# Performance work log

Measured on AMD Instinct MI355X. Metric: run time of the kernel, lower is better.

The kernel has to match this reference:

```python
import jax, jax.numpy as jnp
import numpy as np

MEM = 32      # mem_size == slot_size (required by role/mem einsum contraction)
SLOT = 32
NREAD = 1
NITER = 3
NIN = 3       # num_input
EPS = 1e-8


def _ln(x, g=None, b=None, eps=1e-5):
    m = x.mean(-1, keepdims=True)
    v = x.var(-1, keepdims=True)
    y = (x - m) / jnp.sqrt(v + eps)
    if g is not None:
        y = y * g + b
    return y


def _lstm_layer(x, Wih, Whh, bih, bhh):
    # x: [S, B, Din]; torch gate order i, f, g, o
    B = x.shape[1]
    H = Whh.shape[1]
    def step(carry, xt):
        h, c = carry
        z = xt @ Wih.T + h @ Whh.T + bih + bhh
        i, f, g, o = jnp.split(z, 4, axis=-1)
        c = jax.nn.sigmoid(f) * c + jax.nn.sigmoid(i) * jnp.tanh(g)
        h = jax.nn.sigmoid(o) * jnp.tanh(c)
        return (h, c), h
    init = (jnp.zeros((B, H), x.dtype), jnp.zeros((B, H), x.dtype))
    _, hs = jax.lax.scan(step, init, x)
    return hs


def _slot_attention(inp, inp_cat, Wi, bi, Wq, bq, Wk, bk, Wv, bv, lng, lnb,
                    Wm1, bm1, Wm2, bm2, Wsp, bsp):
    # inp: [S, B, NIN, 64]; dropout is identity (eval)
    S, B = inp.shape[0], inp.shape[1]
    init_slots = (inp_cat @ Wi.T + bi).reshape(S, B, -1, SLOT)
    k = jax.nn.elu(inp @ Wk.T + bk) + 1.0
    v = inp @ Wv.T + bv
    slots = init_slots
    for _ in range(NITER):
        q = (slots @ Wq.T + bq + init_slots) * SLOT ** (-0.5)
        q = jax.nn.elu(q) + 1.0
        logits = jnp.einsum('sbik,sbjk->sbij', k, q)
        attn = jax.nn.softmax(logits, axis=3) + EPS
        attn = attn / attn.sum(axis=2, keepdims=True)
        upd = jnp.einsum('sbij,sbik->sbjk', attn, v)
        h = _ln(upd, lng, lnb)
        mlp = jax.nn.relu(h @ Wm1.T + bm1) @ Wm2.T + bm2
        slots = slots + mlp / SLOT
    slots = jnp.concatenate([init_slots, slots], axis=-1)
    return slots @ Wsp.T + bsp


def _mask_read(slots, mask, i):
    return jnp.tanh(jnp.einsum('sbne,n->sbe', slots, jnp.roll(mask, i)))


def setup_inputs() -> dict:
    key = jax.random.key(0)
    ks = jax.random.split(key, 20)
    def n(k, shape):
        return jax.random.normal(k, shape, jnp.float32) * 0.05
    z = lambda s: jnp.zeros(s, jnp.float32)
    return {
        'tokens': jax.random.randint(ks[0], (512, 64), 0, 32000),
        'embed_W': n(ks[1], (32000, 256)),
        'Wih0': n(ks[2], (2048, 256)), 'Whh0': n(ks[3], (2048, 512)),
        'bih0': z(2048), 'bhh0': z(2048),
        'Wih1': n(ks[4], (2048, 512)), 'Whh1': n(ks[5], (2048, 512)),
        'bih1': z(2048), 'bhh1': z(2048),
        'Wpi': n(ks[6], (192, 256)), 'bpi': z(192),
        'Wq': n(ks[7], (32, 32)), 'bq': z(32),
        'Wk': n(ks[8], (32, 64)), 'bk': z(32),
        'Wv': n(ks[9], (32, 64)), 'bv': z(32),
        'lng': jnp.ones(32, jnp.float32), 'lnb': z(32),
        'Wm1': n(ks[10], (64, 32)), 'bm1': z(64),
        'Wm2': n(ks[11], (32, 64)), 'bm2': z(32),
        'Wbind': n(ks[12], (96, 192)), 'bbind': z(96),
        'Wreas': n(ks[13], (64, 192)), 'breas': z(64),
        'Wsp': n(ks[14], (32, 64)), 'bsp': z(32),
        'Wg': n(ks[15], (1, 512)), 'bg': z(1),
        'Wout': n(ks[16], (128, 544)), 'bout': z(128),
    }


def reference(tokens, embed_W, Wih0, Whh0, bih0, bhh0, Wih1, Whh1, bih1, bhh1,
              Wpi, bpi, Wq, bq, Wk, bk, Wv, bv, lng, lnb, Wm1, bm1, Wm2, bm2,
              Wbind, bbind, Wreas, breas, Wsp, bsp, Wg, bg, Wout, bout):
    S, B = tokens.shape
    emb = embed_W[tokens]                                   # [S,B,256]
    h = _lstm_layer(emb, Wih0, Whh0, bih0, bhh0)            # [S,B,512]
    h = _lstm_layer(h, Wih1, Whh1, bih1, bhh1)
    dec_in = (emb @ Wpi.T + bpi).reshape(S, B, NIN, -1)     # [S,B,3,64]
    dec_cat = dec_in.reshape(S, B, -1)
    sa = (Wq, bq, Wk, bk, Wv, bv, lng, lnb, Wm1, bm1, Wm2, bm2, Wsp, bsp)
    bind_slots = _slot_attention(dec_in, dec_cat, Wbind, bbind, *sa)  # [S,B,3,32]
    reas_slots = _slot_attention(dec_in, dec_cat, Wreas, breas, *sa)  # [S,B,2,32]
    e = 1e-6
    mask_b = jnp.array([1.0 - 2 * e, e, e], emb.dtype)
    role1 = _mask_read(bind_slots, mask_b, 0)
    role2 = _mask_read(bind_slots, mask_b, 1)
    filler = _mask_read(bind_slots, mask_b, 2)
    mask_r = jnp.array([1.0 - (1 + NREAD) * e, e], emb.dtype)
    u1 = _mask_read(reas_slots, mask_r, 0)
    u2 = _mask_read(reas_slots, mask_r, 1)
    gate = jax.nn.sigmoid(h @ Wg.T + bg + 1.0)              # [S,B,1]

    def step(mem, xs):
        r1, r2, f, g_t, u1t, u2t = xs
        role = jnp.einsum('br,bt->brt', r1, r2)
        prev = jnp.einsum('brt,brtf->bf', role, mem)
        cur = g_t * (f - prev)
        mem = mem + jnp.einsum('brt,bf->brtf', role, cur / MEM)
        nrm = jnp.sqrt(jnp.sum(mem * mem, axis=(1, 2, 3)))
        nrm = jax.nn.relu(nrm - 1.0) + 1.0
        mem = mem / nrm[:, None, None, None]
        read = _ln(jnp.einsum('bsrv,bs,br->bv', mem, u1t, u2t))
        return mem, read

    mem0 = jnp.zeros((B, MEM, MEM, MEM), emb.dtype)
    _, reads = jax.lax.scan(step, mem0, (role1, role2, filler, gate, u1, u2))
    out = jnp.concatenate([h, reads], axis=-1) @ Wout.T + bout
    return out
```

## Files before the change

kernel.cpp:

```cpp
#include <hip/hip_runtime.h>

typedef unsigned short u16;
typedef unsigned int u32;
typedef unsigned long long u64;
typedef __bf16 bf16x8 __attribute__((ext_vector_type(8)));
typedef float f32x4 __attribute__((ext_vector_type(4)));

__device__ __forceinline__ float bf2f(u16 u) { return __uint_as_float(((u32)u) << 16); }
__device__ __forceinline__ u16 f2bf(float f) {
    u32 u = __float_as_uint(f);
    u32 r = (u + 0x7FFFu + ((u >> 16) & 1u)) >> 16;
    return (u16)r;
}
__device__ __forceinline__ float sigm(float x) { return 1.0f / (1.0f + __expf(-x)); }
__device__ __forceinline__ float elu1(float x) { return x > 0.0f ? x + 1.0f : __expf(x); }

__device__ __forceinline__ void wb() { __builtin_amdgcn_wave_barrier(); }

__device__ __forceinline__ int ag_load(const int* p) {
    return __hip_atomic_load(p, __ATOMIC_RELAXED, __HIP_MEMORY_SCOPE_AGENT);
}
__device__ __forceinline__ void ag_store(int* p, int v) {
    __hip_atomic_store(p, v, __ATOMIC_RELAXED, __HIP_MEMORY_SCOPE_AGENT);
}
__device__ __forceinline__ void llc_store2(u16* p, u16 a, u16 b) {
    u32 v = (u32)a | ((u32)b << 16);
    __hip_atomic_store((u32*)p, v, __ATOMIC_RELAXED, __HIP_MEMORY_SCOPE_AGENT);
}
__device__ __forceinline__ void llc_store_u16(u16* p, u16 v) {
    __hip_atomic_store(p, v, __ATOMIC_RELAXED, __HIP_MEMORY_SCOPE_AGENT);
}

struct Cvt8 { const float* s[8]; u16* d[8]; int off4[9]; };

__global__ __launch_bounds__(256) void k_f2b8(Cvt8 c)
{
    int i = blockIdx.x * 256 + threadIdx.x;
    if (i >= c.off4[8]) return;
    int k = 0;
#pragma unroll
    for (int q = 1; q < 8; q++) if (i >= c.off4[q]) k = q;
    int j = i - c.off4[k];
    float4 v = ((const float4*)c.s[k])[j];
    ushort4 o;
    o.x = f2bf(v.x); o.y = f2bf(v.y); o.z = f2bf(v.z); o.w = f2bf(v.w);
    ((ushort4*)c.d[k])[j] = o;
}

__global__ __launch_bounds__(256) void k_embed(const int* __restrict__ tok,
                                               const float* __restrict__ W,
                                               u16* __restrict__ out)
{
    int c = blockIdx.x * 256 + threadIdx.x;
    int row = c >> 5, cc = (c & 31) * 8;
    int t = tok[row];
    const float* src = W + (size_t)t * 256 + cc;
    u16 tmp[8];
#pragma unroll
    for (int k = 0; k < 8; k++) tmp[k] = f2bf(src[k]);
    *(uint4*)(out + (size_t)row * 256 + cc) = *(uint4*)tmp;
}

__global__ __launch_bounds__(256) void k_gemm_bt(
    const u16* __restrict__ A, int lda,
    const u16* __restrict__ B,
    u16* __restrict__ Cb, float* __restrict__ Cf, int ldc,
    const float* __restrict__ bias1, const float* __restrict__ bias2,
    int N, int K)
{
    __shared__ u16 As[128][40];
    __shared__ u16 Bs[128][40];
    const int tid = threadIdx.x;
    const int m0 = blockIdx.x * 128, n0 = blockIdx.y * 128;
    const int wave = tid >> 6, lane = tid & 63;
    const int wm = wave & 1, wn = wave >> 1;
    const int quad = lane >> 4, l16 = lane & 15;
    f32x4 acc[4][4] = {};
    for (int k0 = 0; k0 < K; k0 += 32) {
        __syncthreads();
#pragma unroll
        for (int i = 0; i < 2; i++) {
            int c = tid + i * 256, row = c >> 2, cc = (c & 3) * 8;
            *(uint4*)(&As[row][cc]) = *(const uint4*)(A + (size_t)(m0 + row) * lda + k0 + cc);
            uint4 d = {0, 0, 0, 0};
            if (n0 + row < N) d = *(const uint4*)(B + (size_t)(n0 + row) * K + k0 + cc);
            *(uint4*)(&Bs[row][cc]) = d;
        }
        __syncthreads();
        bf16x8 af[4], bfm[4];
#pragma unroll
        for (int x = 0; x < 4; x++) {
            af[x]  = *(const bf16x8*)(&As[wm * 64 + x * 16 + l16][quad * 8]);
            bfm[x] = *(const bf16x8*)(&Bs[wn * 64 + x * 16 + l16][quad * 8]);
        }
#pragma unroll
        for (int mi = 0; mi < 4; mi++)
#pragma unroll
            for (int ni = 0; ni < 4; ni++)
                acc[mi][ni] = __builtin_amdgcn_mfma_f32_16x16x32_bf16(af[mi], bfm[ni], acc[mi][ni], 0, 0, 0);
    }
#pragma unroll
    for (int ni = 0; ni < 4; ni++) {
        int col = n0 + wn * 64 + ni * 16 + l16;
        if (col < N) {
            float bv = 0.f;
            if (bias1) bv += bias1[col];
            if (bias2) bv += bias2[col];
#pragma unroll
            for (int mi = 0; mi < 4; mi++) {
                int r0 = m0 + wm * 64 + mi * 16 + quad * 4;
#pragma unroll
                for (int r = 0; r < 4; r++) {
                    float v = acc[mi][ni][r] + bv;
                    if (Cb) Cb[(size_t)(r0 + r) * ldc + col] = f2bf(v);
                    else    Cf[(size_t)(r0 + r) * ldc + col] = v;
                }
            }
        }
    }
}

struct SmemSlot {
    float WqT[32][33], WkT[64][33], WvT[64][33], Wm1T[32][65], Wm2T[64][33], WspT[64][33];
    float bq[32], bk[32], bv[32], bm1[64], bm2[32], bsp[32], g[32], be[32];
    u16 xbuf[8][192];
    float slots[8][3][32], initl[8][3][32], kk[8][3][32], vv[8][3][32], qq[8][3][32];
    float att[8][3][4];
    float ubuf[8][32];
    float hid[8][64];
};

__device__ __forceinline__ void stage_slot_weights(SmemSlot& S, const int tid,
    const float* __restrict__ Wq, const float* __restrict__ bq,
    const float* __restrict__ Wk, const float* __restrict__ bk,
    const float* __restrict__ Wv, const float* __restrict__ bv,
    const float* __restrict__ lng, const float* __restrict__ lnb,
    const float* __restrict__ Wm1, const float* __restrict__ bm1,
    const float* __restrict__ Wm2, const float* __restrict__ bm2,
    const float* __restrict__ Wsp, const float* __restrict__ bsp)
{
    for (int i = tid; i < 1024; i += 256) { int o = i >> 5, c = i & 31; S.WqT[c][o] = Wq[o * 32 + c]; }
    for (int i = tid; i < 2048; i += 256) {
        int o6 = i >> 6, c6 = i & 63;
        S.WkT[c6][o6]  = Wk[o6 * 64 + c6];
        S.WvT[c6][o6]  = Wv[o6 * 64 + c6];
        S.Wm2T[c6][o6] = Wm2[o6 * 64 + c6];
        S.WspT[c6][o6] = Wsp[o6 * 64 + c6];
        int o5 = i >> 5, c5 = i & 31;
        S.Wm1T[c5][o5] = Wm1[o5 * 32 + c5];
    }
    if (tid < 32) {
        S.bq[tid] = bq[tid]; S.bk[tid] = bk[tid]; S.bv[tid] = bv[tid];
        S.bm2[tid] = bm2[tid]; S.bsp[tid] = bsp[tid];
        S.g[tid] = lng[tid]; S.be[tid] = lnb[tid];
    }
    if (tid < 64) S.bm1[tid] = bm1[tid];
}

template <int NSLOT>
__device__ __forceinline__ void slot_unit(
    SmemSlot& S, const int tid, const size_t row0,
    const u16* __restrict__ dec, const u16* __restrict__ initp,
    float* __restrict__ o1, float* __restrict__ o2, float* __restrict__ o3)
{
    const int p = tid >> 5, l = tid & 31;
    const size_t row = row0 + p;
    for (int i = l; i < 192; i += 32) S.xbuf[p][i] = dec[row * 192 + i];
    wb();
#pragma unroll
    for (int i = 0; i < 3; i++) {
        float k0 = 0.f, k1 = 0.f, v0 = 0.f, v1 = 0.f;
#pragma unroll
        for (int c = 0; c < 64; c += 4) {
            float x0 = bf2f(S.xbuf[p][i * 64 + c]);
            float x1 = bf2f(S.xbuf[p][i * 64 + c + 1]);
            float x2 = bf2f(S.xbuf[p][i * 64 + c + 2]);
            float x3 = bf2f(S.xbuf[p][i * 64 + c + 3]);
            float wk0 = S.WkT[c][l], wk1 = S.WkT[c + 1][l];
            float wk2 = S.WkT[c + 2][l], wk3 = S.WkT[c + 3][l];
            float wv0 = S.WvT[c][l], wv1 = S.WvT[c + 1][l];
            float wv2 = S.WvT[c + 2][l], wv3 = S.WvT[c + 3][l];
            k0 += x0 * wk0; k1 += x1 * wk1; k0 += x2 * wk2; k1 += x3 * wk3;
            v0 += x0 * wv0; v1 += x1 * wv1; v0 += x2 * wv2; v1 += x3 * wv3;
        }
        S.kk[p][i][l] = elu1(S.bk[l] + (k0 + k1));
        S.vv[p][i][l] = S.bv[l] + (v0 + v1);
    }
#pragma unroll
    for (int j = 0; j < NSLOT; j++) {
        float iv = bf2f(initp[row * (NSLOT * 32) + j * 32 + l]);
        S.initl[p][j][l] = iv;
        S.slots[p][j][l] = iv;
    }
    wb();
    const float rs = 0.17677669529663687f;
    for (int it = 0; it < 3; it++) {
#pragma unroll
        for (int j = 0; j < NSLOT; j++) {
            float a0 = 0.f, a1 = 0.f, a2 = 0.f, a3 = 0.f;
#pragma unroll
            for (int c = 0; c < 32; c += 4) {
                float s0 = S.slots[p][j][c],     s1 = S.slots[p][j][c + 1];
                float s2 = S.slots[p][j][c + 2], s3 = S.slots[p][j][c + 3];
                float w0 = S.WqT[c][l],     w1 = S.WqT[c + 1][l];
                float w2 = S.WqT[c + 2][l], w3 = S.WqT[c + 3][l];
                a0 += s0 * w0; a1 += s1 * w1; a2 += s2 * w2; a3 += s3 * w3;
            }
            S.qq[p][j][l] = elu1((S.bq[l] + ((a0 + a1) + (a2 + a3)) + S.initl[p][j][l]) * rs);
        }
        wb();
        if (l < 3 * NSLOT) {
            int i = l / NSLOT, j = l % NSLOT;
            float a0 = 0.f, a1 = 0.f, a2 = 0.f, a3 = 0.f;
#pragma unroll
            for (int c = 0; c < 32; c += 4) {
                a0 += S.kk[p][i][c]     * S.qq[p][j][c];
                a1 += S.kk[p][i][c + 1] * S.qq[p][j][c + 1];
                a2 += S.kk[p][i][c + 2] * S.qq[p][j][c + 2];
                a3 += S.kk[p][i][c + 3] * S.qq[p][j][c + 3];
            }
            S.att[p][i][j] = (a0 + a1) + (a2 + a3);
        }
        wb();
        if (l < 3) {
            float mx = -1e30f;
            for (int j = 0; j < NSLOT; j++) mx = fmaxf(mx, S.att[p][l][j]);
            float sm = 0.f, ex[3];
            for (int j = 0; j < NSLOT; j++) { ex[j] = __expf(S.att[p][l][j] - mx); sm += ex[j]; }
            for (int j = 0; j < NSLOT; j++) S.att[p][l][j] = ex[j] / sm + 1e-8f;
        }
        wb();
        if (l < NSLOT) {
            float s = S.att[p][0][l] + S.att[p][1][l] + S.att[p][2][l];
            float inv = 1.0f / s;
            for (int i = 0; i < 3; i++) S.att[p][i][l] *= inv;
        }
        wb();
#pragma unroll
        for (int j = 0; j < NSLOT; j++) {
            float u = S.att[p][0][j] * S.vv[p][0][l] + S.att[p][1][j] * S.vv[p][1][l] + S.att[p][2][j] * S.vv[p][2][l];
            float mean = u;
            for (int mk = 1; mk < 32; mk <<= 1) mean += __shfl_xor(mean, mk, 32);
            mean *= (1.0f / 32.0f);
            float d = u - mean;
            float var = d * d;
            for (int mk = 1; mk < 32; mk <<= 1) var += __shfl_xor(var, mk, 32);
            var *= (1.0f / 32.0f);
            float y = d * rsqrtf(var + 1e-5f) * S.g[l] + S.be[l];
            S.ubuf[p][l] = y;
            wb();
#pragma unroll
            for (int oo = 0; oo < 2; oo++) {
                int o = l + oo * 32;
                float a0 = 0.f, a1 = 0.f, a2 = 0.f, a3 = 0.f;
#pragma unroll
                for (int c = 0; c < 32; c += 4) {
                    float u0 = S.ubuf[p][c],     u1v_ = S.ubuf[p][c + 1];
                    float u2v_ = S.ubuf[p][c + 2], u3 = S.ubuf[p][c + 3];
                    float w0 = S.Wm1T[c][o],     w1 = S.Wm1T[c + 1][o];
                    float w2 = S.Wm1T[c + 2][o], w3 = S.Wm1T[c + 3][o];
                    a0 += u0 * w0; a1 += u1v_ * w1; a2 += u2v_ * w2; a3 += u3 * w3;
                }
                S.hid[p][o] = fmaxf(S.bm1[o] + ((a0 + a1) + (a2 + a3)), 0.f);
            }
            wb();
            float a0 = 0.f, a1 = 0.f, a2 = 0.f, a3 = 0.f;
#pragma unroll
            for (int c = 0; c < 64; c += 4) {
                float h0 = S.hid[p][c],     h1 = S.hid[p][c + 1];
                float h2 = S.hid[p][c + 2], h3 = S.hid[p][c + 3];
                float w0 = S.Wm2T[c][l],     w1 = S.Wm2T[c + 1][l];
                float w2 = S.Wm2T[c + 2][l], w3 = S.Wm2T[c + 3][l];
                a0 += h0 * w0; a1 += h1 * w1; a2 += h2 * w2; a3 += h3 * w3;
            }
            S.slots[p][j][l] += (S.bm2[l] + ((a0 + a1) + (a2 + a3))) * (1.0f / 32.0f);
            wb();
        }
    }
    float pj[NSLOT];
#pragma unroll
    for (int j = 0; j < NSLOT; j++) {
        float a0 = 0.f, a1 = 0.f, a2 = 0.f, a3 = 0.f;
#pragma unroll
        for (int c = 0; c < 32; c += 4) {
            float i0 = S.initl[p][j][c],     i1 = S.initl[p][j][c + 1];
            float i2 = S.initl[p][j][c + 2], i3 = S.initl[p][j][c + 3];
            float w0 = S.WspT[c][l],     w1 = S.WspT[c + 1][l];
            float w2 = S.WspT[c + 2][l], w3 = S.WspT[c + 3][l];
            a0 += i0 * w0; a1 += i1 * w1; a2 += i2 * w2; a3 += i3 * w3;
        }
#pragma unroll
        for (int c = 0; c < 32; c += 4) {
            float s0 = S.slots[p][j][c],     s1 = S.slots[p][j][c + 1];
            float s2 = S.slots[p][j][c + 2], s3 = S.slots[p][j][c + 3];
            float w0 = S.WspT[32 + c][l],     w1 = S.WspT[32 + c + 1][l];
            float w2 = S.WspT[32 + c + 2][l], w3 = S.WspT[32 + c + 3][l];
            a0 += s0 * w0; a1 += s1 * w1; a2 += s2 * w2; a3 += s3 * w3;
        }
        pj[j] = S.bsp[l] + ((a0 + a1) + (a2 + a3));
    }
    const float e = 1e-6f, me = (float)(1.0 - 2e-6);
    if (NSLOT == 3) {
        o1[row * 32 + l] = tanhf(me * pj[0] + e * pj[1] + e * pj[2]);
        o2[row * 32 + l] = tanhf(e * pj[0] + me * pj[1] + e * pj[2]);
        o3[row * 32 + l] = tanhf(e * pj[0] + e * pj[1] + me * pj[2]);
    } else {
        o1[row * 32 + l] = tanhf(me * pj[0] + e * pj[1]);
        o2[row * 32 + l] = tanhf(e * pj[0] + me * pj[1]);
    }
}

__global__ __launch_bounds__(256) void k_slotsweep(
    const u16* __restrict__ dec,
    const u16* __restrict__ initb, const u16* __restrict__ initr,
    const float* __restrict__ Wq, const float* __restrict__ bq,
    const float* __restrict__ Wk, const float* __restrict__ bk,
    const float* __restrict__ Wv, const float* __restrict__ bv,
    const float* __restrict__ lng, const float* __restrict__ lnb,
    const float* __restrict__ Wm1, const float* __restrict__ bm1,
    const float* __restrict__ Wm2, const float* __restrict__ bm2,
    const float* __restrict__ Wsp, const float* __restrict__ bsp,
    float* __restrict__ r1, float* __restrict__ r2, float* __restrict__ fi,
    float* __restrict__ u1, float* __restrict__ u2)
{
    __shared__ SmemSlot S;
    const int tid = threadIdx.x;
    stage_slot_weights(S, tid, Wq, bq, Wk, bk, Wv, bv, lng, lnb,
                       Wm1, bm1, Wm2, bm2, Wsp, bsp);
    __syncthreads();
    for (int u = blockIdx.x; u < 8192; u += 512) {
        const int t = u >> 4, s = u & 15;
        if (s < 8)
            slot_unit<3>(S, tid, (size_t)t * 64 + s * 8, dec, initb, r1, r2, fi);
        else
            slot_unit<2>(S, tid, (size_t)t * 64 + (s - 8) * 8, dec, initr, u1, u2, nullptr);
        wb();
    }
}

__global__ __launch_bounds__(256) void k_mega(
    const u16* __restrict__ emb,
    const u16* __restrict__ Wx0, const u16* __restrict__ Wh0,
    const u16* __restrict__ Wx1, const u16* __restrict__ Wh1,
    const float* __restrict__ bi0, const float* __restrict__ bh0,
    const float* __restrict__ bi1, const float* __restrict__ bh1,
    u16* __restrict__ h0seq,
    u16* __restrict__ h1seq,
    u16* __restrict__ acat,
    int* __restrict__ flags,
    const float* __restrict__ r1, const float* __restrict__ r2,
    const float* __restrict__ fi, const float* __restrict__ uu1,
    const float* __restrict__ uu2,
    const float* __restrict__ Wg, const float* __restrict__ bg)
{
    const int tid = threadIdx.x;
    const int blk = blockIdx.x;
    int* f0  = flags;
    int* f1  = flags + 4096;
    int* f1s = flags + 8192;

    if (blk < 128) {
        __shared__ u16 Wx[32][528];
        __shared__ u16 Wh[32][528];
        __shared__ float zs[4][16][33];
        const int layer = blk >> 6;
        const int me = blk & 63;
        const int jbase = me * 8;
        const int Kx = layer ? 512 : 256;
        const u16* Wxp = layer ? Wx1 : Wx0;
        const u16* Whp = layer ? Wh1 : Wh0;
        const float* bi = layer ? bi1 : bi0;
        const float* bh = layer ? bh1 : bh0;
#pragma unroll
        for (int i = 0; i < 8; i++) {
            int c = tid + i * 256;
            int row = c >> 6, cc = (c & 63) * 8;
            int grow = (row >> 3) * 512 + jbase + (row & 7);
            *(uint4*)(&Wh[row][cc]) = *(const uint4*)(Whp + (size_t)grow * 512 + cc);
        }
        {
            int cpr = Kx >> 3;
            int iters = (32 * cpr) >> 8;
            for (int i = 0; i < iters; i++) {
                int c = tid + i * 256;
                int row = c / cpr, cc = (c % cpr) * 8;
                int grow = (row >> 3) * 512 + jbase + (row & 7);
                *(uint4*)(&Wx[row][cc]) = *(const uint4*)(Wxp + (size_t)grow * Kx + cc);
            }
        }
        const int wave = tid >> 6, lane = tid & 63;
        const int quad = lane >> 4, l16 = lane & 15;
        const int m = wave * 16 + l16;
        const int bl = lane >> 2;
        const int b = wave * 16 + bl;
        const int jj = (lane & 3) * 2;
        const int hoff = quad * 512 + m * 8;
        float bia0[4], bia1[4];
#pragma unroll
        for (int g = 0; g < 4; g++) {
            bia0[g] = bi[g * 512 + jbase + jj]     + bh[g * 512 + jbase + jj];
            bia1[g] = bi[g * 512 + jbase + jj + 1] + bh[g * 512 + jbase + jj + 1];
        }
        const int pollOwn = (wave * 64 + lane) * 16;
        const int pubIdx  = (wave * 64 + me) * 16;
        float c0 = 0.f, c1 = 0.f;
        __syncthreads();
        for (int t = 0; t < 512; t++) {
            f32x4 acc0 = {}, acc1 = {};
            if (!layer) {
                const u16* xrow = emb + ((size_t)t * 64 + m) * 256;
#pragma unroll
                for (int kc = 0; kc < 8; kc++) {
                    bf16x8 a  = *(const bf16x8*)(xrow + kc * 32 + quad * 8);
                    bf16x8 w0 = *(const bf16x8*)(&Wx[l16][kc * 32 + quad * 8]);
                    bf16x8 w1 = *(const bf16x8*)(&Wx[16 + l16][kc * 32 + quad * 8]);
                    acc0 = __builtin_amdgcn_mfma_f32_16x16x32_bf16(a, w0, acc0, 0, 0, 0);
                    acc1 = __builtin_amdgcn_mfma_f32_16x16x32_bf16(a, w1, acc1, 0, 0, 0);
                }
                if (t > 0) {
                    int it = 0;
                    for (;;) {
                        int a = ag_load(f0 + pollOwn);
                        if (__all(a >= t)) break;
                        if (++it > 3000000) break;
                        __builtin_amdgcn_s_sleep(1);
                    }
                    const u16* hrd = h0seq + (size_t)(t - 1) * 32768 + hoff;
#pragma unroll
                    for (int kc = 0; kc < 16; kc++) {
                        bf16x8 a  = *(const bf16x8*)(hrd + kc * 2048);
                        bf16x8 w0 = *(const bf16x8*)(&Wh[l16][kc * 32 + quad * 8]);
                        bf16x8 w1 = *(const bf16x8*)(&Wh[16 + l16][kc * 32 + quad * 8]);
                        acc0 = __builtin_amdgcn_mfma_f32_16x16x32_bf16(a, w0, acc0, 0, 0, 0);
                        acc1 = __builtin_amdgcn_mfma_f32_16x16x32_bf16(a, w1, acc1, 0, 0, 0);
                    }
                }
            } else {
                {
                    int it = 0;
                    for (;;) {
                        int a = ag_load(f0 + pollOwn);
                        if (__all(a >= t + 1)) break;
                        if (++it > 3000000) break;
                        __builtin_amdgcn_s_sleep(1);
                    }
                }
                const u16* xrow = h0seq + (size_t)t * 32768 + hoff;
#pragma unroll
                for (int kc = 0; kc < 16; kc++) {
                    bf16x8 a  = *(const bf16x8*)(xrow + kc * 2048);
                    bf16x8 w0 = *(const bf16x8*)(&Wx[l16][kc * 32 + quad * 8]);
                    bf16x8 w1 = *(const bf16x8*)(&Wx[16 + l16][kc * 32 + quad * 8]);
                    acc0 = __builtin_amdgcn_mfma_f32_16x16x32_bf16(a, w0, acc0, 0, 0, 0);
                    acc1 = __builtin_amdgcn_mfma_f32_16x16x32_bf16(a, w1, acc1, 0, 0, 0);
                }
                if (t > 0) {
                    int it = 0;
                    for (;;) {
                        int a = ag_load(f1 + pollOwn);
                        if (__all(a >= t)) break;
                        if (++it > 3000000) break;
                        __builtin_amdgcn_s_sleep(1);
                    }
                    const u16* hrd = h1seq + (size_t)(t - 1) * 32768 + hoff;
#pragma unroll
                    for (int kc = 0; kc < 16; kc++) {
                        bf16x8 a  = *(const bf16x8*)(hrd + kc * 2048);
                        bf16x8 w0 = *(const bf16x8*)(&Wh[l16][kc * 32 + quad * 8]);
                        bf16x8 w1 = *(const bf16x8*)(&Wh[16 + l16][kc * 32 + quad * 8]);
                        acc0 = __builtin_amdgcn_mfma_f32_16x16x32_bf16(a, w0, acc0, 0, 0, 0);
                        acc1 = __builtin_amdgcn_mfma_f32_16x16x32_bf16(a, w1, acc1, 0, 0, 0);
                    }
                }
            }
#pragma unroll
            for (int r = 0; r < 4; r++) {
                zs[wave][quad * 4 + r][l16]      = acc0[r];
                zs[wave][quad * 4 + r][16 + l16] = acc1[r];
            }
            u16 hb0, hb1;
            {
                float zi0 = zs[wave][bl][jj]      + bia0[0];
                float zf0 = zs[wave][bl][8 + jj]  + bia0[1];
                float zg0 = zs[wave][bl][16 + jj] + bia0[2];
                float zo0 = zs[wave][bl][24 + jj] + bia0[3];
                c0 = sigm(zf0) * c0 + sigm(zi0) * tanhf(zg0);
                float h0v = sigm(zo0) * tanhf(c0);
                float zi1 = zs[wave][bl][jj + 1]      + bia1[0];
                float zf1 = zs[wave][bl][8 + jj + 1]  + bia1[1];
                float zg1 = zs[wave][bl][16 + jj + 1] + bia1[2];
                float zo1 = zs[wave][bl][24 + jj + 1] + bia1[3];
                c1 = sigm(zf1) * c1 + sigm(zi1) * tanhf(zg1);
                float h1v = sigm(zo1) * tanhf(c1);
                hb0 = f2bf(h0v); hb1 = f2bf(h1v);
            }
            if (!layer) {
                llc_store2(h0seq + (size_t)t * 32768 + me * 512 + b * 8 + jj, hb0, hb1);
                __builtin_amdgcn_s_waitcnt(0);
                if (lane == 0) ag_store(f0 + pubIdx, t + 1);
            } else {
                llc_store2(h1seq + (size_t)t * 32768 + me * 512 + b * 8 + jj, hb0, hb1);
                __builtin_amdgcn_s_waitcnt(0);
                if (lane == 0) ag_store(f1 + pubIdx, t + 1);
                llc_store2(acat + ((size_t)t * 64 + b) * 544 + jbase + jj, hb0, hb1);
                __builtin_amdgcn_s_waitcnt(0);
                if (lane == 0) ag_store(f1s + pubIdx, t + 1);
            }
        }
    } else {
        const int sb = blk - 128;
        const int grp = sb >> 4;
        const int f = tid & 31, rg = tid >> 5;
        float m[4][32];
#pragma unroll
        for (int x = 0; x < 4; x++)
            for (int y = 0; y < 32; y++) m[x][y] = 0.f;
        __shared__ float r1s[32], r2s[32], fis[32], u1s[32], u2s[32];
        __shared__ float red[8][32];
        __shared__ float wred[4];
        __shared__ float gpart[4];
        float wg0 = Wg[2 * tid], wg1 = Wg[2 * tid + 1];
        float bgv = bg[0];
        for (int t = 0; t < 512; t++) {
            float pre = 0.f;
            {
                size_t base = ((size_t)t * 64 + sb) * 32;
                if (tid < 32) pre = r1[base + tid];
                else if (tid < 64) pre = r2[base + tid - 32];
                else if (tid < 96) pre = fi[base + tid - 64];
                else if (tid < 128) pre = uu1[base + tid - 96];
                else if (tid < 160) pre = uu2[base + tid - 128];
            }
            if (tid < 64) {
                int* p1 = f1s + (grp * 64 + tid) * 16;
                int it = 0;
                for (;;) {
                    int a = ag_load(p1);
                    if (__all(a >= t + 1)) break;
                    if (++it > 3000000) break;
                    __builtin_amdgcn_s_sleep(1);
                }
            }
            __syncthreads();
            if (tid < 32) r1s[tid] = pre;
            else if (tid < 64) r2s[tid - 32] = pre;
            else if (tid < 96) fis[tid - 64] = pre;
            else if (tid < 128) u1s[tid - 96] = pre;
            else if (tid < 160) u2s[tid - 128] = pre;
            {
                const u16* hr = acat + ((size_t)t * 64 + sb) * 544;
                u32 hv = *(const u32*)(hr + 2 * tid);
                float gp = bf2f((u16)hv) * wg0 + bf2f((u16)(hv >> 16)) * wg1;
                for (int mk = 1; mk < 64; mk <<= 1) gp += __shfl_xor(gp, mk, 64);
                if ((tid & 63) == 0) gpart[tid >> 6] = gp;
            }
            __syncthreads();
            float gsh = sigm(gpart[0] + gpart[1] + gpart[2] + gpart[3] + bgv + 1.0f);
            float p = 0.f;
#pragma unroll
            for (int rl = 0; rl < 4; rl++) {
                float s = 0.f;
                for (int ti = 0; ti < 32; ti++) s += r2s[ti] * m[rl][ti];
                p += r1s[rg * 4 + rl] * s;
            }
            red[rg][f] = p;
            __syncthreads();
            float prev = 0.f;
#pragma unroll
            for (int g = 0; g < 8; g++) prev += red[g][f];
            float curo = gsh * (fis[f] - prev) * (1.0f / 32.0f);
            float nsq = 0.f;
#pragma unroll
            for (int rl = 0; rl < 4; rl++) {
                float a = r1s[rg * 4 + rl] * curo;
                for (int ti = 0; ti < 32; ti++) {
                    m[rl][ti] += a * r2s[ti];
                    nsq += m[rl][ti] * m[rl][ti];
                }
            }
            for (int mk = 1; mk < 64; mk <<= 1) nsq += __shfl_xor(nsq, mk, 64);
            __syncthreads();
            if ((tid & 63) == 0) wred[tid >> 6] = nsq;
            __syncthreads();
            float nrm = sqrtf(wred[0] + wred[1] + wred[2] + wred[3]);
            float sc = nrm > 1.0f ? 1.0f / nrm : 1.0f;
            float rp = 0.f;
#pragma unroll
            for (int rl = 0; rl < 4; rl++) {
                float s = 0.f;
                for (int ti = 0; ti < 32; ti++) {
                    m[rl][ti] *= sc;
                    s += m[rl][ti] * u2s[ti];
                }
                rp += u1s[rg * 4 + rl] * s;
            }
            red[rg][f] = rp;
            __syncthreads();
            float rv = 0.f;
#pragma unroll
            for (int g = 0; g < 8; g++) rv += red[g][f];
            float mean = rv;
            for (int mk = 1; mk < 32; mk <<= 1) mean += __shfl_xor(mean, mk, 32);
            mean *= (1.0f / 32.0f);
            float d = rv - mean;
            float var = d * d;
            for (int mk = 1; mk < 32; mk <<= 1) var += __shfl_xor(var, mk, 32);
            var *= (1.0f / 32.0f);
            if (tid < 32) {
                float y = d * rsqrtf(var + 1e-5f);
                llc_store_u16(acat + ((size_t)t * 64 + sb) * 544 + 512 + f, f2bf(y));
            }
            __syncthreads();
        }
    }
}

extern "C" void kernel_launch(void* const* d_in, const int* in_sizes, int n_in,
                              void* d_out, int out_size, void* d_ws, size_t ws_size,
                              hipStream_t stream)
{
    (void)in_sizes; (void)n_in; (void)out_size; (void)ws_size;
    const int*   tokens = (const int*)d_in[0];
    const float* embW  = (const float*)d_in[1];
    const float* Wih0  = (const float*)d_in[2];
    const float* Whh0  = (const float*)d_in[3];
    const float* bih0  = (const float*)d_in[4];
    const float* bhh0  = (const float*)d_in[5];
    const float* Wih1  = (const float*)d_in[6];
    const float* Whh1  = (const float*)d_in[7];
    const float* bih1  = (const float*)d_in[8];
    const float* bhh1  = (const float*)d_in[9];
    const float* Wpi   = (const float*)d_in[10];
    const float* bpi   = (const float*)d_in[11];
    const float* Wq    = (const float*)d_in[12];
    const float* bq    = (const float*)d_in[13];
    const float* Wk    = (const float*)d_in[14];
    const float* bk    = (const float*)d_in[15];
    const float* Wv    = (const float*)d_in[16];
    const float* bv    = (const float*)d_in[17];
    const float* lng   = (const float*)d_in[18];
    const float* lnb   = (const float*)d_in[19];
    const float* Wm1   = (const float*)d_in[20];
    const float* bm1   = (const float*)d_in[21];
    const float* Wm2   = (const float*)d_in[22];
    const float* bm2   = (const float*)d_in[23];
    const float* Wbind = (const float*)d_in[24];
    const float* bbind = (const float*)d_in[25];
    const float* Wreas = (const float*)d_in[26];
    const float* breas = (const float*)d_in[27];
    const float* Wsp   = (const float*)d_in[28];
    const float* bsp   = (const float*)d_in[29];
    const float* Wg    = (const float*)d_in[30];
    const float* bg    = (const float*)d_in[31];
    const float* Wout  = (const float*)d_in[32];
    const float* bout  = (const float*)d_in[33];

    char* ws = (char*)d_ws;
    size_t off = 0;
    auto alloc = [&](size_t bytes) { size_t o = off; off += (bytes + 255) & ~(size_t)255; return o; };
    int*  flags  = (int*)(ws + alloc(16384 * 4));
    u16*  emb    = (u16*)(ws + alloc(32768ull * 256 * 2));
    u16*  dec    = (u16*)(ws + alloc(32768ull * 192 * 2));
    u16*  initb  = (u16*)(ws + alloc(32768ull * 96 * 2));
    u16*  initr  = (u16*)(ws + alloc(32768ull * 64 * 2));
    u16*  acat   = (u16*)(ws + alloc(32768ull * 544 * 2));
    u16*  h0seq  = (u16*)(ws + alloc(512ull * 64 * 512 * 2));
    u16*  h1seq  = (u16*)(ws + alloc(512ull * 64 * 512 * 2));
    float* role1 = (float*)(ws + alloc(32768ull * 32 * 4));
    float* role2 = (float*)(ws + alloc(32768ull * 32 * 4));
    float* fill  = (float*)(ws + alloc(32768ull * 32 * 4));
    float* u1v   = (float*)(ws + alloc(32768ull * 32 * 4));
    float* u2v   = (float*)(ws + alloc(32768ull * 32 * 4));
    u16* Wx0b  = (u16*)(ws + alloc(2048ull * 256 * 2));
    u16* Wh0b  = (u16*)(ws + alloc(2048ull * 512 * 2));
    u16* Wx1b  = (u16*)(ws + alloc(2048ull * 512 * 2));
    u16* Wh1b  = (u16*)(ws + alloc(2048ull * 512 * 2));
    u16* Wpib  = (u16*)(ws + alloc(192ull * 256 * 2));
    u16* Wbindb = (u16*)(ws + alloc(96ull * 192 * 2));
    u16* Wreasb = (u16*)(ws + alloc(64ull * 192 * 2));
    u16* Woutb  = (u16*)(ws + alloc(128ull * 544 * 2));

    hipMemsetAsync(flags, 0, 16384 * 4, stream);
    {
        Cvt8 c;
        const float* s[8] = {Wih0, Whh0, Wih1, Whh1, Wpi, Wbind, Wreas, Wout};
        u16* d[8] = {Wx0b, Wh0b, Wx1b, Wh1b, Wpib, Wbindb, Wreasb, Woutb};
        int n[8] = {2048 * 256, 2048 * 512, 2048 * 512, 2048 * 512,
                    192 * 256, 96 * 192, 64 * 192, 128 * 544};
        int acc = 0;
        for (int k = 0; k < 8; k++) { c.s[k] = s[k]; c.d[k] = d[k]; c.off4[k] = acc; acc += n[k] / 4; }
        c.off4[8] = acc;
        k_f2b8<<<(acc + 255) / 256, 256, 0, stream>>>(c);
    }
    k_embed<<<4096, 256, 0, stream>>>(tokens, embW, emb);
    k_gemm_bt<<<dim3(256, 2), 256, 0, stream>>>(emb, 256, Wpib, dec, nullptr, 192, bpi, nullptr, 192, 256);
    k_gemm_bt<<<dim3(256, 1), 256, 0, stream>>>(dec, 192, Wbindb, initb, nullptr, 96, bbind, nullptr, 96, 192);
    k_gemm_bt<<<dim3(256, 1), 256, 0, stream>>>(dec, 192, Wreasb, initr, nullptr, 64, breas, nullptr, 64, 192);
    k_slotsweep<<<512, 256, 0, stream>>>(dec, initb, initr,
                                         Wq, bq, Wk, bk, Wv, bv, lng, lnb,
                                         Wm1, bm1, Wm2, bm2, Wsp, bsp,
                                         role1, role2, fill, u1v, u2v);
    k_mega<<<192, 256, 0, stream>>>(emb, Wx0b, Wh0b, Wx1b, Wh1b,
                                    bih0, bhh0, bih1, bhh1,
                                    h0seq, h1seq, acat, flags,
                                    role1, role2, fill, u1v, u2v, Wg, bg);
    k_gemm_bt<<<dim3(256, 1), 256, 0, stream>>>(acat, 544, Woutb, nullptr, (float*)d_out, 128, bout, nullptr, 128, 544);
}
```

Before: 3.517 ms.

## Overlap tail of slot-attention sweep with the recurrent megakernel via progress flags

The slot-attention precompute kernel now handles only the first PRE_T timesteps. The remaining units are processed by 63 extra blocks added to the persistent megakernel, which publish per-block progress counters with agent-scope stores. Scan blocks wait on those counters before reading role/filler/read vectors for later timesteps. This hides slot-attention work behind the serial LSTM/memory recurrence, at the cost of more spin-wait polling, a larger grid, and shared memory overlaid in a union.

After: 3.412 ms. 3.0% less time.

```diff
diff --git a/kernel.cpp b/kernel.cpp
--- a/kernel.cpp
+++ b/kernel.cpp
@@ -23,6 +23,9 @@
 __device__ __forceinline__ void ag_store(int* p, int v) {
     __hip_atomic_store(p, v, __ATOMIC_RELAXED, __HIP_MEMORY_SCOPE_AGENT);
 }
+__device__ __forceinline__ void ag_storef(float* p, float v) {
+    __hip_atomic_store(p, v, __ATOMIC_RELAXED, __HIP_MEMORY_SCOPE_AGENT);
+}
 __device__ __forceinline__ void llc_store2(u16* p, u16 a, u16 b) {
     u32 v = (u32)a | ((u32)b << 16);
     __hip_atomic_store((u32*)p, v, __ATOMIC_RELAXED, __HIP_MEMORY_SCOPE_AGENT);
@@ -30,6 +33,9 @@
 __device__ __forceinline__ void llc_store_u16(u16* p, u16 v) {
     __hip_atomic_store(p, v, __ATOMIC_RELAXED, __HIP_MEMORY_SCOPE_AGENT);
 }
+
+#define PRE_T 160
+#define PRE_U (PRE_T * 16)
 
 struct Cvt8 { const float* s[8]; u16* d[8]; int off4[9]; };
 
@@ -120,6 +126,11 @@
     }
 }
 
+struct SmemLstm {
+    u16 Wx[32][528];
+    u16 Wh[32][528];
+    float zs[4][16][33];
+};
 struct SmemSlot {
     float WqT[32][33], WkT[64][33], WvT[64][33], Wm1T[32][65], Wm2T[64][33], WspT[64][33];
     float bq[32], bk[32], bv[32], bm1[64], bm2[32], bsp[32], g[32], be[32];
@@ -128,6 +139,17 @@
     float att[8][3][4];
     float ubuf[8][32];
     float hid[8][64];
+};
+struct SmemScan {
+    float r1s[32], r2s[32], fis[32], u1s[32], u2s[32];
+    float red[8][32];
+    float wred[4];
+    float gpart[4];
+};
+union SmemU {
+    SmemLstm l;
+    SmemSlot s;
+    SmemScan c;
 };
 
 __device__ __forceinline__ void stage_slot_weights(SmemSlot& S, const int tid,
@@ -157,7 +179,7 @@
     if (tid < 64) S.bm1[tid] = bm1[tid];
 }
 
-template <int NSLOT>
+template <int NSLOT, bool LLC>
 __device__ __forceinline__ void slot_unit(
     SmemSlot& S, const int tid, const size_t row0,
     const u16* __restrict__ dec, const u16* __restrict__ initp,
@@ -301,12 +323,16 @@
     }
     const float e = 1e-6f, me = (float)(1.0 - 2e-6);
     if (NSLOT == 3) {
-        o1[row * 32 + l] = tanhf(me * pj[0] + e * pj[1] + e * pj[2]);
-        o2[row * 32 + l] = tanhf(e * pj[0] + me * pj[1] + e * pj[2]);
-        o3[row * 32 + l] = tanhf(e * pj[0] + e * pj[1] + me * pj[2]);
+        float v1 = tanhf(me * pj[0] + e * pj[1] + e * pj[2]);
+        float v2 = tanhf(e * pj[0] + me * pj[1] + e * pj[2]);
+        float v3 = tanhf(e * pj[0] + e * pj[1] + me * pj[2]);
+        if (LLC) { ag_storef(&o1[row * 32 + l], v1); ag_storef(&o2[row * 32 + l], v2); ag_storef(&o3[row * 32 + l], v3); }
+        else     { o1[row * 32 + l] = v1; o2[row * 32 + l] = v2; o3[row * 32 + l] = v3; }
     } else {
-        o1[row * 32 + l] = tanhf(me * pj[0] + e * pj[1]);
-        o2[row * 32 + l] = tanhf(e * pj[0] + me * pj[1]);
+        float v1 = tanhf(me * pj[0] + e * pj[1]);
+        float v2 = tanhf(e * pj[0] + me * pj[1]);
+        if (LLC) { ag_storef(&o1[row * 32 + l], v1); ag_storef(&o2[row * 32 + l], v2); }
+        else     { o1[row * 32 + l] = v1; o2[row * 32 + l] = v2; }
     }
 }
 
@@ -328,12 +354,12 @@
     stage_slot_weights(S, tid, Wq, bq, Wk, bk, Wv, bv, lng, lnb,
                        Wm1, bm1, Wm2, bm2, Wsp, bsp);
     __syncthreads();
-    for (int u = blockIdx.x; u < 8192; u += 512) {
+    for (int u = blockIdx.x; u < PRE_U; u += 512) {
         const int t = u >> 4, s = u & 15;
         if (s < 8)
-            slot_unit<3>(S, tid, (size_t)t * 64 + s * 8, dec, initb, r1, r2, fi);
+            slot_unit<3, false>(S, tid, (size_t)t * 64 + s * 8, dec, initb, r1, r2, fi);
         else
-            slot_unit<2>(S, tid, (size_t)t * 64 + (s - 8) * 8, dec, initr, u1, u2, nullptr);
+            slot_unit<2, false>(S, tid, (size_t)t * 64 + (s - 8) * 8, dec, initr, u1, u2, nullptr);
         wb();
     }
 }
@@ -348,21 +374,31 @@
     u16* __restrict__ h1seq,
     u16* __restrict__ acat,
     int* __restrict__ flags,
-    const float* __restrict__ r1, const float* __restrict__ r2,
-    const float* __restrict__ fi, const float* __restrict__ uu1,
-    const float* __restrict__ uu2,
-    const float* __restrict__ Wg, const float* __restrict__ bg)
+    float* __restrict__ r1, float* __restrict__ r2,
+    float* __restrict__ fi, float* __restrict__ uu1, float* __restrict__ uu2,
+    const float* __restrict__ Wg, const float* __restrict__ bg,
+    const u16* __restrict__ dec,
+    const u16* __restrict__ initb, const u16* __restrict__ initr,
+    const float* __restrict__ Wq, const float* __restrict__ bq,
+    const float* __restrict__ Wk, const float* __restrict__ bk,
+    const float* __restrict__ Wv, const float* __restrict__ bv,
+    const float* __restrict__ lng, const float* __restrict__ lnb,
+    const float* __restrict__ Wm1, const float* __restrict__ bm1,
+    const float* __restrict__ Wm2, const float* __restrict__ bm2,
+    const float* __restrict__ Wsp, const float* __restrict__ bsp)
 {
+    __shared__ SmemU sm;
     const int tid = threadIdx.x;
     const int blk = blockIdx.x;
-    int* f0  = flags;
-    int* f1  = flags + 4096;
-    int* f1s = flags + 8192;
+    int* f0   = flags;
+    int* f1   = flags + 4096;
+    int* f1s  = flags + 8192;
+    int* prog = flags + 12288;
 
     if (blk < 128) {
-        __shared__ u16 Wx[32][528];
-        __shared__ u16 Wh[32][528];
-        __shared__ float zs[4][16][33];
+        auto& Wx = sm.l.Wx;
+        auto& Wh = sm.l.Wh;
+        auto& zs = sm.l.zs;
         const int layer = blk >> 6;
         const int me = blk & 63;
         const int jbase = me * 8;
@@ -507,7 +543,7 @@
                 if (lane == 0) ag_store(f1s + pubIdx, t + 1);
             }
         }
-    } else {
+    } else if (blk < 192) {
         const int sb = blk - 128;
         const int grp = sb >> 4;
         const int f = tid & 31, rg = tid >> 5;
@@ -515,13 +551,40 @@
 #pragma unroll
         for (int x = 0; x < 4; x++)
             for (int y = 0; y < 32; y++) m[x][y] = 0.f;
-        __shared__ float r1s[32], r2s[32], fis[32], u1s[32], u2s[32];
-        __shared__ float red[8][32];
-        __shared__ float wred[4];
-        __shared__ float gpart[4];
+        auto& r1s = sm.c.r1s;
+        auto& r2s = sm.c.r2s;
+        auto& fis = sm.c.fis;
+        auto& u1s = sm.c.u1s;
+        auto& u2s = sm.c.u2s;
+        auto& red = sm.c.red;
+        auto& wred = sm.c.wred;
+        auto& gpart = sm.c.gpart;
         float wg0 = Wg[2 * tid], wg1 = Wg[2 * tid + 1];
         float bgv = bg[0];
         for (int t = 0; t < 512; t++) {
+            if (tid < 64) {
+                int* p1 = f1s + (grp * 64 + tid) * 16;
+                int it = 0;
+                for (;;) {
+                    int a = ag_load(p1);
+                    if (__all(a >= t + 1)) break;
+                    if (++it > 3000000) break;
+                    __builtin_amdgcn_s_sleep(1);
+                }
+            } else if (tid < 128 && t >= PRE_T) {
+                const int k = tid - 64;
+                const int* pp = prog + k * 16;
+                const int need = (t + 1) * 16;
+                int it = 0;
+                for (;;) {
+                    int a = 0x7FFFFFFF;
+                    if (k < 63) a = ag_load(pp);
+                    if (__all(a >= need)) break;
+                    if (++it > 3000000) break;
+                    __builtin_amdgcn_s_sleep(1);
+                }
+            }
+            __syncthreads();
             float pre = 0.f;
             {
                 size_t base = ((size_t)t * 64 + sb) * 32;
@@ -531,22 +594,6 @@
                 else if (tid < 128) pre = uu1[base + tid - 96];
                 else if (tid < 160) pre = uu2[base + tid - 128];
             }
-            if (tid < 64) {
-                int* p1 = f1s + (grp * 64 + tid) * 16;
-                int it = 0;
-                for (;;) {
-                    int a = ag_load(p1);
-                    if (__all(a >= t + 1)) break;
-                    if (++it > 3000000) break;
-                    __builtin_amdgcn_s_sleep(1);
-                }
-            }
-            __syncthreads();
-            if (tid < 32) r1s[tid] = pre;
-            else if (tid < 64) r2s[tid - 32] = pre;
-            else if (tid < 96) fis[tid - 64] = pre;
-            else if (tid < 128) u1s[tid - 96] = pre;
-            else if (tid < 160) u2s[tid - 128] = pre;
             {
                 const u16* hr = acat + ((size_t)t * 64 + sb) * 544;
                 u32 hv = *(const u32*)(hr + 2 * tid);
@@ -554,6 +601,11 @@
                 for (int mk = 1; mk < 64; mk <<= 1) gp += __shfl_xor(gp, mk, 64);
                 if ((tid & 63) == 0) gpart[tid >> 6] = gp;
             }
+            if (tid < 32) r1s[tid] = pre;
+            else if (tid < 64) r2s[tid - 32] = pre;
+            else if (tid < 96) fis[tid - 64] = pre;
+            else if (tid < 128) u1s[tid - 96] = pre;
+            else if (tid < 160) u2s[tid - 128] = pre;
             __syncthreads();
             float gsh = sigm(gpart[0] + gpart[1] + gpart[2] + gpart[3] + bgv + 1.0f);
             float p = 0.f;
@@ -611,6 +663,22 @@
                 llc_store_u16(acat + ((size_t)t * 64 + sb) * 544 + 512 + f, f2bf(y));
             }
             __syncthreads();
+        }
+    } else {
+        const int wid = blk - 192;
+        stage_slot_weights(sm.s, tid, Wq, bq, Wk, bk, Wv, bv, lng, lnb,
+                           Wm1, bm1, Wm2, bm2, Wsp, bsp);
+        __syncthreads();
+        int* myprog = prog + wid * 16;
+        for (int u = PRE_U + wid; u < 8192; u += 63) {
+            const int t = u >> 4, s = u & 15;
+            if (s < 8)
+                slot_unit<3, true>(sm.s, tid, (size_t)t * 64 + s * 8, dec, initb, r1, r2, fi);
+            else
+                slot_unit<2, true>(sm.s, tid, (size_t)t * 64 + (s - 8) * 8, dec, initr, uu1, uu2, nullptr);
+            __builtin_amdgcn_s_waitcnt(0);
+            __syncthreads();
+            if (tid == 0) ag_store(myprog, u + 63);
         }
     }
 }
@@ -700,9 +768,12 @@
                                          Wq, bq, Wk, bk, Wv, bv, lng, lnb,
                                          Wm1, bm1, Wm2, bm2, Wsp, bsp,
                                          role1, role2, fill, u1v, u2v);
-    k_mega<<<192, 256, 0, stream>>>(emb, Wx0b, Wh0b, Wx1b, Wh1b,
+    k_mega<<<255, 256, 0, stream>>>(emb, Wx0b, Wh0b, Wx1b, Wh1b,
                                     bih0, bhh0, bih1, bhh1,
                                     h0seq, h1seq, acat, flags,
-                                    role1, role2, fill, u1v, u2v, Wg, bg);
+                                    role1, role2, fill, u1v, u2v, Wg, bg,
+                                    dec, initb, initr,
+                                    Wq, bq, Wk, bk, Wv, bv, lng, lnb,
+                                    Wm1, bm1, Wm2, bm2, Wsp, bsp);
     k_gemm_bt<<<dim3(256, 1), 256, 0, stream>>>(acat, 544, Woutb, nullptr, (float*)d_out, 128, bout, nullptr, 128, 544);
 }
```
